# Kernel tuning notes

Measured on AMD Instinct MI355X. Metric: run time of the kernel, lower is better.

Reference implementation:

```python
import jax, jax.numpy as jnp
import numpy as np
from jax import lax

B, N, SEG, T = 64, 19, 15, 400
FIN, HID, K, NH, DM, FF, L, NC = 64, 128, 4, 4, 64, 128, 4, 3
EPS = 1e-5


def setup_inputs() -> dict:
    key = jax.random.key(0)
    ks = jax.random.split(key, 40)
    nrm = lambda i, s, sc=0.05: jax.random.normal(ks[i], s, dtype=jnp.float32) * sc
    inp = {
        "X": jax.random.normal(ks[0], (B, N, SEG, T), dtype=jnp.float32),
        "A_hat": jax.random.uniform(ks[1], (B, K, SEG, N, N), dtype=jnp.float32),
        "conv1_w": nrm(2, (32, 1, 25)), "conv1_b": nrm(3, (32,)),
        "conv2_w": nrm(4, (64, 32, 9)), "conv2_b": nrm(5, (64,)),
        "g1_W": nrm(6, (HID, FIN)), "g1_q": nrm(7, (K,), 1.0),
        "g1_bn_g": jnp.ones((HID,)), "g1_bn_b": jnp.zeros((HID,)),
        "g1_bn_m": jnp.zeros((HID,)), "g1_bn_v": jnp.ones((HID,)),
        "g2_W": nrm(8, (FIN, HID)), "g2_q": nrm(9, (K,), 1.0),
        "g2_bn_g": jnp.ones((FIN,)), "g2_bn_b": jnp.zeros((FIN,)),
        "g2_bn_m": jnp.zeros((FIN,)), "g2_bn_v": jnp.ones((FIN,)),
        "cls_token": nrm(10, (1, 1, DM), 0.02), "pos_emb": nrm(11, (1, SEG + 1, DM), 0.02),
        "t_wqkv": nrm(12, (L, 3 * DM, DM)), "t_bqkv": nrm(13, (L, 3 * DM)),
        "t_wo": nrm(14, (L, DM, DM)), "t_bo": nrm(15, (L, DM)),
        "t_ln1g": jnp.ones((L, DM)), "t_ln1b": jnp.zeros((L, DM)),
        "t_w1": nrm(16, (L, FF, DM)), "t_b1": nrm(17, (L, FF)),
        "t_w2": nrm(18, (L, DM, FF)), "t_b2": nrm(19, (L, DM)),
        "t_ln2g": jnp.ones((L, DM)), "t_ln2b": jnp.zeros((L, DM)),
        "clf_w": nrm(20, (NC, DM)), "clf_b": nrm(21, (NC,)),
    }
    return inp


def _ln(x, g, b):
    mu = x.mean(-1, keepdims=True)
    v = ((x - mu) ** 2).mean(-1, keepdims=True)
    return (x - mu) * lax.rsqrt(v + EPS) * g + b


def _maxpool(x, w):  # x: [M, C, T]
    return lax.reduce_window(x, -jnp.inf, lax.max, (1, 1, w), (1, 1, w), "VALID")


def _temporal_encoder(X, c1w, c1b, c2w, c2b):
    # X: [B, SEG, N, T] -> [B, SEG, N, FIN]
    x = X.reshape(-1, 1, T)
    dn = ("NCH", "OIH", "NCH")
    x = lax.conv_general_dilated(x, c1w, (4,), [(12, 12)], dimension_numbers=dn) + c1b[None, :, None]
    x = _maxpool(jax.nn.relu(x), 4)                      # [M,32,25]
    x = lax.conv_general_dilated(x, c2w, (2,), [(4, 4)], dimension_numbers=dn) + c2b[None, :, None]
    x = _maxpool(jax.nn.relu(x), 2)                      # [M,64,6]
    x = x.mean(-1)                                       # AdaptiveAvgPool1d(1)
    return x.reshape(B, SEG, N, FIN)


def _gcn(Xf, A, W, q, g, b, m, v):
    alpha = jax.nn.softmax(q)                            # [K]
    AX = jnp.einsum("bksnm,bsmf->bksnf", A, Xf)          # K-hop diffusion
    Hk = jnp.einsum("bksnf,of->bksno", AX, W)            # shared linear
    H = jnp.einsum("k,bksno->bsno", alpha, Hk)           # attn-weighted hop mix
    H = (H - m) * lax.rsqrt(v + EPS) * g + b             # eval-mode BatchNorm1d
    return jax.nn.relu(H)


def _forward(X, A_hat, conv1_w, conv1_b, conv2_w, conv2_b,
             g1_W, g1_q, g1_bn_g, g1_bn_b, g1_bn_m, g1_bn_v,
             g2_W, g2_q, g2_bn_g, g2_bn_b, g2_bn_m, g2_bn_v,
             cls_token, pos_emb, t_wqkv, t_bqkv, t_wo, t_bo,
             t_ln1g, t_ln1b, t_w1, t_b1, t_w2, t_b2, t_ln2g, t_ln2b,
             clf_w, clf_b):
    Xs = X.reshape(-1, N, SEG, T).transpose(0, 2, 1, 3)  # [B,SEG,N,T]
    feat = _temporal_encoder(Xs, conv1_w, conv1_b, conv2_w, conv2_b)
    H = _gcn(feat, A_hat, g1_W, g1_q, g1_bn_g, g1_bn_b, g1_bn_m, g1_bn_v)
    H = _gcn(H, A_hat, g2_W, g2_q, g2_bn_g, g2_bn_b, g2_bn_m, g2_bn_v)
    g = H.mean(axis=2)                                   # node-mean -> [B,SEG,DM]
    x = jnp.concatenate([jnp.broadcast_to(cls_token, (B, 1, DM)), g], axis=1)
    x = x + pos_emb[:, : SEG + 1]
    dh = DM // NH
    for l in range(L):
        qkv = x @ t_wqkv[l].T + t_bqkv[l]
        qh, kh, vh = [u.reshape(B, SEG + 1, NH, dh).transpose(0, 2, 1, 3)
                      for u in jnp.split(qkv, 3, axis=-1)]
        attn = jax.nn.softmax(jnp.einsum("bhqd,bhkd->bhqk", qh, kh) / jnp.sqrt(jnp.float32(dh)), axis=-1)
        o = jnp.einsum("bhqk,bhkd->bhqd", attn, vh).transpose(0, 2, 1, 3).reshape(B, SEG + 1, DM)
        x = _ln(x + o @ t_wo[l].T + t_bo[l], t_ln1g[l], t_ln1b[l])
        ff = jax.nn.relu(x @ t_w1[l].T + t_b1[l]) @ t_w2[l].T + t_b2[l]
        x = _ln(x + ff, t_ln2g[l], t_ln2b[l])
    return x[:, 0] @ clf_w.T + clf_b                     # [B, NC]


def reference(X, A_hat, conv1_w, conv1_b, conv2_w, conv2_b,
              g1_W, g1_q, g1_bn_g, g1_bn_b, g1_bn_m, g1_bn_v,
              g2_W, g2_q, g2_bn_g, g2_bn_b, g2_bn_m, g2_bn_v,
              cls_token, pos_emb, t_wqkv, t_bqkv, t_wo, t_bo,
              t_ln1g, t_ln1b, t_w1, t_b1, t_w2, t_b2, t_ln2g, t_ln2b,
              clf_w, clf_b):
    return _forward(X, A_hat, conv1_w, conv1_b, conv2_w, conv2_b,
                    g1_W, g1_q, g1_bn_g, g1_bn_b, g1_bn_m, g1_bn_v,
                    g2_W, g2_q, g2_bn_g, g2_bn_b, g2_bn_m, g2_bn_v,
                    cls_token, pos_emb, t_wqkv, t_bqkv, t_wo, t_bo,
                    t_ln1g, t_ln1b, t_w1, t_b1, t_w2, t_b2, t_ln2g, t_ln2b,
                    clf_w, clf_b)
```

## Files before the change

kernel.cpp:

```cpp
#include <hip/hip_runtime.h>
#include <cmath>

#define B_ 64
#define N_ 19
#define SEG_ 15
#define T_ 400
#define FIN_ 64
#define HID_ 128
#define K_ 4
#define NH_ 4
#define DM_ 64
#define FF_ 128
#define L_ 4
#define NC_ 3
#define EPS_ 1e-5f

typedef __attribute__((ext_vector_type(8))) short bf16x8;
typedef __attribute__((ext_vector_type(4))) short bf16x4;
typedef __attribute__((ext_vector_type(4))) float f32x4;
typedef unsigned short ushort_t;

__device__ __forceinline__ ushort_t f2bf(float x) {
  union { float f; unsigned u; } a; a.f = x;
  unsigned r = a.u + 0x7fffu + ((a.u >> 16) & 1u);
  return (ushort_t)(r >> 16);
}
__device__ __forceinline__ float bf2f(ushort_t h) {
  union { unsigned u; float f; } a; a.u = ((unsigned)h) << 16;
  return a.f;
}

__global__ __launch_bounds__(256) void k_prep(
    const float* __restrict__ c1w, const float* __restrict__ c2w,
    const float* __restrict__ wqkv, const float* __restrict__ wo,
    const float* __restrict__ w1, const float* __restrict__ w2,
    const float* __restrict__ g1W, const float* __restrict__ g2W,
    ushort_t* __restrict__ bt,
    ushort_t* __restrict__ Th, ushort_t* __restrict__ Tl,
    ushort_t* __restrict__ W1h, ushort_t* __restrict__ W1l,
    ushort_t* __restrict__ W2h, ushort_t* __restrict__ W2l,
    ushort_t* __restrict__ C1h, ushort_t* __restrict__ C1l) {
  int gid = blockIdx.x * 256 + threadIdx.x;
  if (gid < 18944) {
    int oc = gid / 296, k = gid - oc * 296;
    int ic = k & 31, kk = k >> 5;
    ushort_t v = 0;
    if (kk < 9) v = f2bf(c2w[oc * 288 + ic * 9 + kk]);
    bt[gid] = v;
  } else if (gid < 68096) {
    int i = gid - 18944;
    int l = i / 12288, r = i % 12288;
    float v = wqkv[i];
    ushort_t h = f2bf(v);
    int dst = l * 32768 + r;
    Th[dst] = h; Tl[dst] = f2bf(v - bf2f(h));
  } else if (gid < 84480) {
    int i = gid - 68096;
    int l = i / 4096, r = i % 4096;
    float v = wo[i];
    ushort_t h = f2bf(v);
    int dst = l * 32768 + 12288 + r;
    Th[dst] = h; Tl[dst] = f2bf(v - bf2f(h));
  } else if (gid < 117248) {
    int i = gid - 84480;
    int l = i / 8192, r = i % 8192;
    float v = w1[i];
    ushort_t h = f2bf(v);
    int dst = l * 32768 + 16384 + r;
    Th[dst] = h; Tl[dst] = f2bf(v - bf2f(h));
  } else if (gid < 150016) {
    int i = gid - 117248;
    int l = i / 8192, r = i % 8192;
    float v = w2[i];
    ushort_t h = f2bf(v);
    int dst = l * 32768 + 24576 + r;
    Th[dst] = h; Tl[dst] = f2bf(v - bf2f(h));
  } else if (gid < 158208) {
    int i = gid - 150016;
    float v = g1W[i];
    ushort_t h = f2bf(v);
    W1h[i] = h;
    W1l[i] = f2bf(v - bf2f(h));
  } else if (gid < 166400) {
    int i = gid - 158208;
    float v = g2W[i];
    ushort_t h = f2bf(v);
    W2h[i] = h;
    W2l[i] = f2bf(v - bf2f(h));
  } else if (gid < 167424) {
    int i = gid - 166400;
    int oc = i >> 5, kk = i & 31;
    float v = (kk < 25) ? c1w[oc * 25 + kk] : 0.f;
    ushort_t h = f2bf(v);
    C1h[i] = h;
    C1l[i] = f2bf(v - bf2f(h));
  }
}

#define RPB 4
#define ICP 40
#define P1R 40
#define OFF_XPH 0
#define OFF_XPL 3840
#define OFF_P1  7680
#define SMEM_T  20480

__global__ __launch_bounds__(256, 4) void k_temporal(
    const float* __restrict__ X, const float* __restrict__ c1b,
    const float* __restrict__ c2b,
    const ushort_t* __restrict__ C1h, const ushort_t* __restrict__ C1l,
    const ushort_t* __restrict__ BmatT, float* __restrict__ Xf) {
  __shared__ __align__(16) unsigned char smem[SMEM_T];
  ushort_t* xph = (ushort_t*)(smem + OFF_XPH);
  ushort_t* xpl = (ushort_t*)(smem + OFF_XPL);
  ushort_t* p1T = (ushort_t*)(smem + OFF_P1);
  float* Dbuf = (float*)smem;

  const int tid = threadIdx.x;
  const int row0 = blockIdx.x * RPB;
  const int lane = tid & 63, wv = tid >> 6;
  const int quad = lane >> 4, nl = lane & 15;

  for (int i = tid; i < 3200; i += 256) ((unsigned*)p1T)[i] = 0u;
  for (int r = 0; r < RPB; ++r) {
    const int gr = row0 + r;
    const int n = gr % N_;
    const int s = (gr / N_) % SEG_;
    const int b = gr / (N_ * SEG_);
    const float* xin = X + (((size_t)b * N_ + n) * SEG_ + s) * T_ - 12;
    for (int i = tid; i < 480; i += 256) {
      float v = (i >= 12 && i < 412) ? xin[i] : 0.f;
      ushort_t h = f2bf(v);
      xph[r * 480 + i] = h;
      xpl[r * 480 + i] = f2bf(v - bf2f(h));
    }
  }
  __syncthreads();

  {
    bf16x8 bh0 = *(const bf16x8*)(C1h + nl * 32 + quad * 8);
    bf16x8 bh1 = *(const bf16x8*)(C1h + (16 + nl) * 32 + quad * 8);
    bf16x8 bl0 = *(const bf16x8*)(C1l + nl * 32 + quad * 8);
    bf16x8 bl1 = *(const bf16x8*)(C1l + (16 + nl) * 32 + quad * 8);
    const float bias0 = c1b[nl], bias1 = c1b[16 + nl];
    for (int t = wv; t < 28; t += 4) {
      const int r = t / 7, mt = t - r * 7;
      const int aoff = r * 480 + mt * 64 + nl * 4 + quad * 8;
      union { bf16x4 q[2]; bf16x8 v; } ah, al;
      ah.q[0] = *(const bf16x4*)(xph + aoff);
      ah.q[1] = *(const bf16x4*)(xph + aoff + 4);
      al.q[0] = *(const bf16x4*)(xpl + aoff);
      al.q[1] = *(const bf16x4*)(xpl + aoff + 4);
      f32x4 a0 = (f32x4){0.f, 0.f, 0.f, 0.f};
      a0 = __builtin_amdgcn_mfma_f32_16x16x32_bf16(ah.v, bh0, a0, 0, 0, 0);
      a0 = __builtin_amdgcn_mfma_f32_16x16x32_bf16(al.v, bh0, a0, 0, 0, 0);
      a0 = __builtin_amdgcn_mfma_f32_16x16x32_bf16(ah.v, bl0, a0, 0, 0, 0);
      f32x4 a1 = (f32x4){0.f, 0.f, 0.f, 0.f};
      a1 = __builtin_amdgcn_mfma_f32_16x16x32_bf16(ah.v, bh1, a1, 0, 0, 0);
      a1 = __builtin_amdgcn_mfma_f32_16x16x32_bf16(al.v, bh1, a1, 0, 0, 0);
      a1 = __builtin_amdgcn_mfma_f32_16x16x32_bf16(ah.v, bl1, a1, 0, 0, 0);
      const int j = mt * 4 + quad;
      if (j < 25) {
        float m0 = fmaxf(fmaxf(a0[0], a0[1]), fmaxf(a0[2], a0[3]));
        float m1 = fmaxf(fmaxf(a1[0], a1[1]), fmaxf(a1[2], a1[3]));
        p1T[(r * P1R + j + 4) * ICP + nl] = f2bf(fmaxf(m0 + bias0, 0.f));
        p1T[(r * P1R + j + 4) * ICP + 16 + nl] = f2bf(fmaxf(m1 + bias1, 0.f));
      }
    }
  }
  __syncthreads();

  f32x4 acc[4];
  int abase[4];
#pragma unroll
  for (int tm = 0; tm < 4; ++tm) {
    acc[tm] = (f32x4){0.f, 0.f, 0.f, 0.f};
    int m = tm * 16 + nl;
    int rl = m / 14;
    int op = m - rl * 14;
    if (rl > 3) rl = 3;
    if (op > 13) op = 13;
    abase[tm] = (rl * P1R + 2 * op) * ICP + quad * 8;
  }
  const ushort_t* brow = BmatT + (wv * 16 + nl) * 296 + quad * 8;
#pragma unroll
  for (int kk = 0; kk < 9; ++kk) {
    bf16x8 bfr = *(const bf16x8*)(brow + kk * 32);
#pragma unroll
    for (int tm = 0; tm < 4; ++tm) {
      bf16x8 afr = *(const bf16x8*)(p1T + abase[tm] + kk * ICP);
      acc[tm] = __builtin_amdgcn_mfma_f32_16x16x32_bf16(afr, bfr, acc[tm], 0, 0, 0);
    }
  }
  __syncthreads();

#pragma unroll
  for (int tm = 0; tm < 4; ++tm)
#pragma unroll
    for (int rg = 0; rg < 4; ++rg)
      Dbuf[(tm * 16 + quad * 4 + rg) * 66 + wv * 16 + nl] = acc[tm][rg];
  __syncthreads();

  for (int o = tid; o < RPB * 64; o += 256) {
    int rl = o >> 6, oc = o & 63;
    float bias = c2b[oc];
    const float* dr = Dbuf + (rl * 14) * 66 + oc;
    float s = 0.f;
#pragma unroll
    for (int jj = 0; jj < 6; ++jj) {
      float v = fmaxf(dr[(2 * jj) * 66], dr[(2 * jj + 1) * 66]) + bias;
      s += fmaxf(v, 0.f);
    }
    Xf[(size_t)(row0 + rl) * FIN_ + oc] = s * (1.f / 6.f);
  }
}

__global__ __launch_bounds__(256, 2) void k_gcn(
    const float* __restrict__ A, const float* __restrict__ Xf,
    const ushort_t* __restrict__ W1h, const ushort_t* __restrict__ W1l,
    const ushort_t* __restrict__ W2h, const ushort_t* __restrict__ W2l,
    const float* __restrict__ q1, const float* __restrict__ q2,
    const float* __restrict__ b1g, const float* __restrict__ b1b,
    const float* __restrict__ b1m, const float* __restrict__ b1v,
    const float* __restrict__ b2g, const float* __restrict__ b2b,
    const float* __restrict__ b2m, const float* __restrict__ b2v,
    float* __restrict__ G) {
  const int bs = blockIdx.x;
  const int b = bs / SEG_;
  const int s = bs % SEG_;
  const int tid = threadIdx.x;
  const int lane = tid & 63, wv = tid >> 6;
  const int quad = lane >> 4, nl = lane & 15;

  __shared__ __align__(16) ushort_t xh[32 * 72], xl[32 * 72];
  __shared__ __align__(16) ushort_t Hh[32 * 136], Hl[32 * 136];
  __shared__ __align__(16) ushort_t a1h[32 * 40], a1l[32 * 40];
  __shared__ __align__(16) ushort_t a2h[32 * 40], a2l[32 * 40];
  __shared__ __align__(16) ushort_t yTh[128 * 40], yTl[128 * 40];
  __shared__ float zbuf[N_ * 64];
  __shared__ float sc1[HID_], sh1[HID_], sc2[FIN_], sh2[FIN_];

  for (int i = tid; i < 32 * 72 / 2; i += 256) {
    ((unsigned*)xh)[i] = 0u; ((unsigned*)xl)[i] = 0u;
  }
  for (int i = tid; i < 32 * 136 / 2; i += 256) {
    ((unsigned*)Hh)[i] = 0u; ((unsigned*)Hl)[i] = 0u;
  }
  for (int i = tid; i < 32 * 40 / 2; i += 256) {
    ((unsigned*)a1h)[i] = 0u; ((unsigned*)a1l)[i] = 0u;
    ((unsigned*)a2h)[i] = 0u; ((unsigned*)a2l)[i] = 0u;
  }
  for (int o = tid; o < HID_; o += 256) {
    float sc = b1g[o] * rsqrtf(b1v[o] + EPS_);
    sc1[o] = sc; sh1[o] = b1b[o] - b1m[o] * sc;
  }
  for (int o = tid; o < FIN_; o += 256) {
    float sc = b2g[o] * rsqrtf(b2v[o] + EPS_);
    sc2[o] = sc; sh2[o] = b2b[o] - b2m[o] * sc;
  }
  __syncthreads();

  {
    float p0 = q1[0], p1 = q1[1], p2 = q1[2], p3 = q1[3];
    float mx = fmaxf(fmaxf(p0, p1), fmaxf(p2, p3));
    float e0 = expf(p0 - mx), e1 = expf(p1 - mx), e2 = expf(p2 - mx), e3 = expf(p3 - mx);
    float inv = 1.f / (e0 + e1 + e2 + e3);
    float a0 = e0 * inv, a1 = e1 * inv, a2 = e2 * inv, a3 = e3 * inv;
    float r0 = q2[0], r1 = q2[1], r2 = q2[2], r3 = q2[3];
    float mx2 = fmaxf(fmaxf(r0, r1), fmaxf(r2, r3));
    float f0 = expf(r0 - mx2), f1 = expf(r1 - mx2), f2 = expf(r2 - mx2), f3 = expf(r3 - mx2);
    float inv2 = 1.f / (f0 + f1 + f2 + f3);
    float c0 = f0 * inv2, c1 = f1 * inv2, c2 = f2 * inv2, c3 = f3 * inv2;
    const size_t kstride = (size_t)SEG_ * N_ * N_;
    const float* Ab = A + ((size_t)b * K_ * SEG_ + s) * (N_ * N_);
    for (int i = tid; i < N_ * N_; i += 256) {
      int n = i / N_, m = i - n * N_;
      float v0 = Ab[i], v1 = Ab[i + kstride], v2 = Ab[i + 2 * kstride], v3 = Ab[i + 3 * kstride];
      float w1v = a0 * v0 + a1 * v1 + a2 * v2 + a3 * v3;
      float w2v = c0 * v0 + c1 * v1 + c2 * v2 + c3 * v3;
      ushort_t h1 = f2bf(w1v);
      a1h[n * 40 + m] = h1; a1l[n * 40 + m] = f2bf(w1v - bf2f(h1));
      ushort_t h2 = f2bf(w2v);
      a2h[n * 40 + m] = h2; a2l[n * 40 + m] = f2bf(w2v - bf2f(h2));
    }
  }
  {
    const float* xb = Xf + (size_t)bs * N_ * FIN_;
    for (int i = tid; i < N_ * FIN_; i += 256) {
      int r = i >> 6, f = i & 63;
      float v = xb[i];
      ushort_t h = f2bf(v);
      xh[r * 72 + f] = h;
      xl[r * 72 + f] = f2bf(v - bf2f(h));
    }
  }
  __syncthreads();

#pragma unroll
  for (int mtl = 0; mtl < 2; ++mtl) {
    const int om = (wv * 2 + mtl) * 16;
#pragma unroll
    for (int nt = 0; nt < 2; ++nt) {
      f32x4 acc = (f32x4){0.f, 0.f, 0.f, 0.f};
#pragma unroll
      for (int ks = 0; ks < 2; ++ks) {
        bf16x8 ah = *(const bf16x8*)(W1h + (om + nl) * 64 + ks * 32 + quad * 8);
        bf16x8 al = *(const bf16x8*)(W1l + (om + nl) * 64 + ks * 32 + quad * 8);
        bf16x8 bh = *(const bf16x8*)(xh + (nt * 16 + nl) * 72 + ks * 32 + quad * 8);
        bf16x8 bl = *(const bf16x8*)(xl + (nt * 16 + nl) * 72 + ks * 32 + quad * 8);
        acc = __builtin_amdgcn_mfma_f32_16x16x32_bf16(ah, bh, acc, 0, 0, 0);
        acc = __builtin_amdgcn_mfma_f32_16x16x32_bf16(al, bh, acc, 0, 0, 0);
        acc = __builtin_amdgcn_mfma_f32_16x16x32_bf16(ah, bl, acc, 0, 0, 0);
      }
#pragma unroll
      for (int r = 0; r < 4; ++r) {
        int o = om + quad * 4 + r, node = nt * 16 + nl;
        float v = acc[r];
        ushort_t hh = f2bf(v);
        yTh[o * 40 + node] = hh;
        yTl[o * 40 + node] = f2bf(v - bf2f(hh));
      }
    }
  }
  __syncthreads();

#pragma unroll
  for (int mt = 0; mt < 2; ++mt) {
#pragma unroll
    for (int ntl = 0; ntl < 2; ++ntl) {
      const int nt = wv * 2 + ntl;
      f32x4 acc = (f32x4){0.f, 0.f, 0.f, 0.f};
      bf16x8 ah = *(const bf16x8*)(a1h + (mt * 16 + nl) * 40 + quad * 8);
      bf16x8 al = *(const bf16x8*)(a1l + (mt * 16 + nl) * 40 + quad * 8);
      bf16x8 bh = *(const bf16x8*)(yTh + (nt * 16 + nl) * 40 + quad * 8);
      bf16x8 bl = *(const bf16x8*)(yTl + (nt * 16 + nl) * 40 + quad * 8);
      acc = __builtin_amdgcn_mfma_f32_16x16x32_bf16(ah, bh, acc, 0, 0, 0);
      acc = __builtin_amdgcn_mfma_f32_16x16x32_bf16(al, bh, acc, 0, 0, 0);
      acc = __builtin_amdgcn_mfma_f32_16x16x32_bf16(ah, bl, acc, 0, 0, 0);
      const int o = nt * 16 + nl;
      const float sc = sc1[o], sh = sh1[o];
#pragma unroll
      for (int r = 0; r < 4; ++r) {
        int node = mt * 16 + quad * 4 + r;
        if (node < N_) {
          float h = fmaxf(acc[r] * sc + sh, 0.f);
          ushort_t hh = f2bf(h);
          Hh[node * 136 + o] = hh;
          Hl[node * 136 + o] = f2bf(h - bf2f(hh));
        }
      }
    }
  }
  __syncthreads();

  {
    const int om = wv * 16;
#pragma unroll
    for (int nt = 0; nt < 2; ++nt) {
      f32x4 acc = (f32x4){0.f, 0.f, 0.f, 0.f};
#pragma unroll
      for (int ks = 0; ks < 4; ++ks) {
        bf16x8 ah = *(const bf16x8*)(W2h + (om + nl) * 128 + ks * 32 + quad * 8);
        bf16x8 al = *(const bf16x8*)(W2l + (om + nl) * 128 + ks * 32 + quad * 8);
        bf16x8 bh = *(const bf16x8*)(Hh + (nt * 16 + nl) * 136 + ks * 32 + quad * 8);
        bf16x8 bl = *(const bf16x8*)(Hl + (nt * 16 + nl) * 136 + ks * 32 + quad * 8);
        acc = __builtin_amdgcn_mfma_f32_16x16x32_bf16(ah, bh, acc, 0, 0, 0);
        acc = __builtin_amdgcn_mfma_f32_16x16x32_bf16(al, bh, acc, 0, 0, 0);
        acc = __builtin_amdgcn_mfma_f32_16x16x32_bf16(ah, bl, acc, 0, 0, 0);
      }
#pragma unroll
      for (int r = 0; r < 4; ++r) {
        int o2 = om + quad * 4 + r, node = nt * 16 + nl;
        float v = acc[r];
        ushort_t hh = f2bf(v);
        yTh[o2 * 40 + node] = hh;
        yTl[o2 * 40 + node] = f2bf(v - bf2f(hh));
      }
    }
  }
  __syncthreads();

#pragma unroll
  for (int mt = 0; mt < 2; ++mt) {
    f32x4 acc = (f32x4){0.f, 0.f, 0.f, 0.f};
    bf16x8 ah = *(const bf16x8*)(a2h + (mt * 16 + nl) * 40 + quad * 8);
    bf16x8 al = *(const bf16x8*)(a2l + (mt * 16 + nl) * 40 + quad * 8);
    bf16x8 bh = *(const bf16x8*)(yTh + (wv * 16 + nl) * 40 + quad * 8);
    bf16x8 bl = *(const bf16x8*)(yTl + (wv * 16 + nl) * 40 + quad * 8);
    acc = __builtin_amdgcn_mfma_f32_16x16x32_bf16(ah, bh, acc, 0, 0, 0);
    acc = __builtin_amdgcn_mfma_f32_16x16x32_bf16(al, bh, acc, 0, 0, 0);
    acc = __builtin_amdgcn_mfma_f32_16x16x32_bf16(ah, bl, acc, 0, 0, 0);
    const int o2 = wv * 16 + nl;
    const float sc = sc2[o2], sh = sh2[o2];
#pragma unroll
    for (int r = 0; r < 4; ++r) {
      int node = mt * 16 + quad * 4 + r;
      if (node < N_)
        zbuf[node * 64 + o2] = fmaxf(acc[r] * sc + sh, 0.f);
    }
  }
  __syncthreads();

  if (tid < FIN_) {
    float ssum = 0.f;
#pragma unroll
    for (int nn = 0; nn < N_; ++nn) ssum += zbuf[nn * 64 + tid];
    G[(size_t)bs * FIN_ + tid] = ssum * (1.f / (float)N_);
  }
}

__global__ __launch_bounds__(256, 1) void k_transformer(
    const float* __restrict__ G, const float* __restrict__ cls,
    const float* __restrict__ pos,
    const ushort_t* __restrict__ Th, const ushort_t* __restrict__ Tl,
    const float* __restrict__ bqkv, const float* __restrict__ bo,
    const float* __restrict__ ln1g, const float* __restrict__ ln1b,
    const float* __restrict__ b1, const float* __restrict__ b2,
    const float* __restrict__ ln2g, const float* __restrict__ ln2b,
    const float* __restrict__ clfw, const float* __restrict__ clfb,
    float* __restrict__ out) {
  const int b = blockIdx.x;
  const int tid = threadIdx.x;
  const int lane = tid & 63, wv = tid >> 6;
  const int quad = lane >> 4, nl = lane & 15;

  __shared__ float xbuf[16 * 64];
  __shared__ __align__(16) ushort_t xh[16 * 72], xl[16 * 72];
  __shared__ float qkvb[16 * 196];
  __shared__ float scb[NH_ * 272];
  __shared__ __align__(16) ushort_t oh[16 * 72], ol[16 * 72];
  __shared__ __align__(16) ushort_t h1h[16 * 136], h1l[16 * 136];
  __shared__ float tmpb[16 * 64];
  __shared__ __align__(16) float pbuf[L_ * 704];
  __shared__ __align__(16) float cw[200];

  for (int i = tid; i < L_ * 704; i += 256) {
    int l = i / 704, r = i - l * 704;
    float v;
    if (r < 192)       v = bqkv[l * 192 + r];
    else if (r < 256)  v = bo[l * 64 + r - 192];
    else if (r < 384)  v = b1[l * 128 + r - 256];
    else if (r < 448)  v = b2[l * 64 + r - 384];
    else if (r < 512)  v = ln1g[l * 64 + r - 448];
    else if (r < 576)  v = ln1b[l * 64 + r - 512];
    else if (r < 640)  v = ln2g[l * 64 + r - 576];
    else               v = ln2b[l * 64 + r - 640];
    pbuf[i] = v;
  }
  if (tid < 192) cw[tid] = clfw[tid];
  if (tid < NC_) cw[192 + tid] = clfb[tid];

  for (int i = tid; i < 16 * 64; i += 256) {
    int t = i >> 6, d = i & 63;
    float base = (t == 0) ? cls[d] : G[((size_t)b * SEG_ + (t - 1)) * DM_ + d];
    float v = base + pos[t * DM_ + d];
    xbuf[i] = v;
    ushort_t h = f2bf(v);
    xh[t * 72 + d] = h;
    xl[t * 72 + d] = f2bf(v - bf2f(h));
  }
  __syncthreads();

  for (int l = 0; l < L_; ++l) {
    const ushort_t* TH = Th + l * 32768;
    const ushort_t* TL = Tl + l * 32768;
    const float* P = pbuf + l * 704;

    bf16x8 qwh[3][2], qwl[3][2];
#pragma unroll
    for (int ntl = 0; ntl < 3; ++ntl)
#pragma unroll
      for (int ks = 0; ks < 2; ++ks) {
        const int nt = wv * 3 + ntl;
        qwh[ntl][ks] = *(const bf16x8*)(TH + (nt * 16 + nl) * 64 + ks * 32 + quad * 8);
        qwl[ntl][ks] = *(const bf16x8*)(TL + (nt * 16 + nl) * 64 + ks * 32 + quad * 8);
      }
    bf16x8 owh[2], owl[2];
#pragma unroll
    for (int ks = 0; ks < 2; ++ks) {
      owh[ks] = *(const bf16x8*)(TH + 12288 + (wv * 16 + nl) * 64 + ks * 32 + quad * 8);
      owl[ks] = *(const bf16x8*)(TL + 12288 + (wv * 16 + nl) * 64 + ks * 32 + quad * 8);
    }
    bf16x8 f1h[2][2], f1l[2][2];
#pragma unroll
    for (int ntl = 0; ntl < 2; ++ntl)
#pragma unroll
      for (int ks = 0; ks < 2; ++ks) {
        const int nt = wv * 2 + ntl;
        f1h[ntl][ks] = *(const bf16x8*)(TH + 16384 + (nt * 16 + nl) * 64 + ks * 32 + quad * 8);
        f1l[ntl][ks] = *(const bf16x8*)(TL + 16384 + (nt * 16 + nl) * 64 + ks * 32 + quad * 8);
      }
    bf16x8 f2h[4], f2l[4];
#pragma unroll
    for (int ks = 0; ks < 4; ++ks) {
      f2h[ks] = *(const bf16x8*)(TH + 24576 + (wv * 16 + nl) * 128 + ks * 32 + quad * 8);
      f2l[ks] = *(const bf16x8*)(TL + 24576 + (wv * 16 + nl) * 128 + ks * 32 + quad * 8);
    }

#pragma unroll
    for (int ntl = 0; ntl < 3; ++ntl) {
      const int nt = wv * 3 + ntl;
      f32x4 acc = (f32x4){0.f, 0.f, 0.f, 0.f};
#pragma unroll
      for (int ks = 0; ks < 2; ++ks) {
        bf16x8 ah = *(const bf16x8*)(xh + nl * 72 + ks * 32 + quad * 8);
        bf16x8 al = *(const bf16x8*)(xl + nl * 72 + ks * 32 + quad * 8);
        acc = __builtin_amdgcn_mfma_f32_16x16x32_bf16(ah, qwh[ntl][ks], acc, 0, 0, 0);
        acc = __builtin_amdgcn_mfma_f32_16x16x32_bf16(al, qwh[ntl][ks], acc, 0, 0, 0);
        acc = __builtin_amdgcn_mfma_f32_16x16x32_bf16(ah, qwl[ntl][ks], acc, 0, 0, 0);
      }
      const int j = nt * 16 + nl;
      const float bias = P[j];
#pragma unroll
      for (int r = 0; r < 4; ++r)
        qkvb[(quad * 4 + r) * 196 + j] = acc[r] + bias;
    }
    __syncthreads();

    {
      const int h = wv;
      float sc[4];
      const float* qr = &qkvb[nl * 196 + h * 16];
#pragma unroll
      for (int uu = 0; uu < 4; ++uu) {
        const float* kr = &qkvb[(quad * 4 + uu) * 196 + 64 + h * 16];
        float a = 0.f;
#pragma unroll
        for (int d = 0; d < 16; ++d) a += qr[d] * kr[d];
        sc[uu] = a * 0.25f;
      }
      float mx = fmaxf(fmaxf(sc[0], sc[1]), fmaxf(sc[2], sc[3]));
      mx = fmaxf(mx, __shfl_xor(mx, 16));
      mx = fmaxf(mx, __shfl_xor(mx, 32));
      float e[4];
      float sum = 0.f;
#pragma unroll
      for (int uu = 0; uu < 4; ++uu) { e[uu] = expf(sc[uu] - mx); sum += e[uu]; }
      sum += __shfl_xor(sum, 16);
      sum += __shfl_xor(sum, 32);
      const float is = 1.f / sum;
      float* prow = &scb[h * 272 + nl * 17];
#pragma unroll
      for (int uu = 0; uu < 4; ++uu) prow[quad * 4 + uu] = e[uu] * is;
      float o[4] = {0.f, 0.f, 0.f, 0.f};
      for (int u = 0; u < 16; ++u) {
        float p = prow[u];
        const float* vr = &qkvb[u * 196 + 128 + h * 16 + quad * 4];
#pragma unroll
        for (int dd = 0; dd < 4; ++dd) o[dd] += p * vr[dd];
      }
      const int eb = h * 16 + quad * 4;
#pragma unroll
      for (int dd = 0; dd < 4; ++dd) {
        ushort_t hh = f2bf(o[dd]);
        oh[nl * 72 + eb + dd] = hh;
        ol[nl * 72 + eb + dd] = f2bf(o[dd] - bf2f(hh));
      }
    }
    __syncthreads();

    {
      f32x4 acc = (f32x4){0.f, 0.f, 0.f, 0.f};
#pragma unroll
      for (int ks = 0; ks < 2; ++ks) {
        bf16x8 ah = *(const bf16x8*)(oh + nl * 72 + ks * 32 + quad * 8);
        bf16x8 al = *(const bf16x8*)(ol + nl * 72 + ks * 32 + quad * 8);
        acc = __builtin_amdgcn_mfma_f32_16x16x32_bf16(ah, owh[ks], acc, 0, 0, 0);
        acc = __builtin_amdgcn_mfma_f32_16x16x32_bf16(al, owh[ks], acc, 0, 0, 0);
        acc = __builtin_amdgcn_mfma_f32_16x16x32_bf16(ah, owl[ks], acc, 0, 0, 0);
      }
      const int d = wv * 16 + nl;
      const float bias = P[192 + d];
#pragma unroll
      for (int r = 0; r < 4; ++r) {
        int t = quad * 4 + r;
        tmpb[t * 64 + d] = xbuf[t * 64 + d] + acc[r] + bias;
      }
    }
    __syncthreads();

    {
      int t = tid >> 4, i2 = tid & 15;
      float4 v = ((const float4*)(tmpb + t * 64))[i2];
      float s = v.x + v.y + v.z + v.w;
      s += __shfl_xor(s, 1); s += __shfl_xor(s, 2);
      s += __shfl_xor(s, 4); s += __shfl_xor(s, 8);
      float mu = s * (1.f / 64.f);
      float d0 = v.x - mu, d1 = v.y - mu, d2 = v.z - mu, d3 = v.w - mu;
      float vr = d0 * d0 + d1 * d1 + d2 * d2 + d3 * d3;
      vr += __shfl_xor(vr, 1); vr += __shfl_xor(vr, 2);
      vr += __shfl_xor(vr, 4); vr += __shfl_xor(vr, 8);
      float rs = rsqrtf(vr * (1.f / 64.f) + EPS_);
      float4 g4 = ((const float4*)(P + 448))[i2];
      float4 b4 = ((const float4*)(P + 512))[i2];
      float4 o4;
      o4.x = d0 * rs * g4.x + b4.x; o4.y = d1 * rs * g4.y + b4.y;
      o4.z = d2 * rs * g4.z + b4.z; o4.w = d3 * rs * g4.w + b4.w;
      ((float4*)(xbuf + t * 64))[i2] = o4;
      int base = t * 72 + i2 * 4;
      ushort_t h0 = f2bf(o4.x), h1 = f2bf(o4.y), h2 = f2bf(o4.z), h3 = f2bf(o4.w);
      xh[base + 0] = h0; xh[base + 1] = h1; xh[base + 2] = h2; xh[base + 3] = h3;
      xl[base + 0] = f2bf(o4.x - bf2f(h0));
      xl[base + 1] = f2bf(o4.y - bf2f(h1));
      xl[base + 2] = f2bf(o4.z - bf2f(h2));
      xl[base + 3] = f2bf(o4.w - bf2f(h3));
    }
    __syncthreads();

#pragma unroll
    for (int ntl = 0; ntl < 2; ++ntl) {
      const int nt = wv * 2 + ntl;
      f32x4 acc = (f32x4){0.f, 0.f, 0.f, 0.f};
#pragma unroll
      for (int ks = 0; ks < 2; ++ks) {
        bf16x8 ah = *(const bf16x8*)(xh + nl * 72 + ks * 32 + quad * 8);
        bf16x8 al = *(const bf16x8*)(xl + nl * 72 + ks * 32 + quad * 8);
        acc = __builtin_amdgcn_mfma_f32_16x16x32_bf16(ah, f1h[ntl][ks], acc, 0, 0, 0);
        acc = __builtin_amdgcn_mfma_f32_16x16x32_bf16(al, f1h[ntl][ks], acc, 0, 0, 0);
        acc = __builtin_amdgcn_mfma_f32_16x16x32_bf16(ah, f1l[ntl][ks], acc, 0, 0, 0);
      }
      const int f = nt * 16 + nl;
      const float bias = P[256 + f];
#pragma unroll
      for (int r = 0; r < 4; ++r) {
        int t = quad * 4 + r;
        float v = fmaxf(acc[r] + bias, 0.f);
        ushort_t hh = f2bf(v);
        h1h[t * 136 + f] = hh;
        h1l[t * 136 + f] = f2bf(v - bf2f(hh));
      }
    }
    __syncthreads();

    {
      f32x4 acc = (f32x4){0.f, 0.f, 0.f, 0.f};
#pragma unroll
      for (int ks = 0; ks < 4; ++ks) {
        bf16x8 ah = *(const bf16x8*)(h1h + nl * 136 + ks * 32 + quad * 8);
        bf16x8 al = *(const bf16x8*)(h1l + nl * 136 + ks * 32 + quad * 8);
        acc = __builtin_amdgcn_mfma_f32_16x16x32_bf16(ah, f2h[ks], acc, 0, 0, 0);
        acc = __builtin_amdgcn_mfma_f32_16x16x32_bf16(al, f2h[ks], acc, 0, 0, 0);
        acc = __builtin_amdgcn_mfma_f32_16x16x32_bf16(ah, f2l[ks], acc, 0, 0, 0);
      }
      const int d = wv * 16 + nl;
      const float bias = P[384 + d];
#pragma unroll
      for (int r = 0; r < 4; ++r) {
        int t = quad * 4 + r;
        tmpb[t * 64 + d] = xbuf[t * 64 + d] + acc[r] + bias;
      }
    }
    __syncthreads();

    {
      int t = tid >> 4, i2 = tid & 15;
      float4 v = ((const float4*)(tmpb + t * 64))[i2];
      float s = v.x + v.y + v.z + v.w;
      s += __shfl_xor(s, 1); s += __shfl_xor(s, 2);
      s += __shfl_xor(s, 4); s += __shfl_xor(s, 8);
      float mu = s * (1.f / 64.f);
      float d0 = v.x - mu, d1 = v.y - mu, d2 = v.z - mu, d3 = v.w - mu;
      float vr = d0 * d0 + d1 * d1 + d2 * d2 + d3 * d3;
      vr += __shfl_xor(vr, 1); vr += __shfl_xor(vr, 2);
      vr += __shfl_xor(vr, 4); vr += __shfl_xor(vr, 8);
      float rs = rsqrtf(vr * (1.f / 64.f) + EPS_);
      float4 g4 = ((const float4*)(P + 576))[i2];
      float4 b4 = ((const float4*)(P + 640))[i2];
      float4 o4;
      o4.x = d0 * rs * g4.x + b4.x; o4.y = d1 * rs * g4.y + b4.y;
      o4.z = d2 * rs * g4.z + b4.z; o4.w = d3 * rs * g4.w + b4.w;
      ((float4*)(xbuf + t * 64))[i2] = o4;
      int base = t * 72 + i2 * 4;
      ushort_t h0 = f2bf(o4.x), h1 = f2bf(o4.y), h2 = f2bf(o4.z), h3 = f2bf(o4.w);
      xh[base + 0] = h0; xh[base + 1] = h1; xh[base + 2] = h2; xh[base + 3] = h3;
      xl[base + 0] = f2bf(o4.x - bf2f(h0));
      xl[base + 1] = f2bf(o4.y - bf2f(h1));
      xl[base + 2] = f2bf(o4.z - bf2f(h2));
      xl[base + 3] = f2bf(o4.w - bf2f(h3));
    }
    __syncthreads();
  }

  if (tid < NC_) {
    float acc = cw[192 + tid];
    const float* wr = &cw[tid * DM_];
    for (int d = 0; d < DM_; ++d) acc += xbuf[d] * wr[d];
    out[b * NC_ + tid] = acc;
  }
}

extern "C" void kernel_launch(void* const* d_in, const int* in_sizes, int n_in,
                              void* d_out, int out_size, void* d_ws, size_t ws_size,
                              hipStream_t stream) {
  (void)in_sizes; (void)n_in; (void)out_size; (void)ws_size;
  const float* X    = (const float*)d_in[0];
  const float* A    = (const float*)d_in[1];
  const float* c1w  = (const float*)d_in[2];
  const float* c1b  = (const float*)d_in[3];
  const float* c2w  = (const float*)d_in[4];
  const float* c2b  = (const float*)d_in[5];
  const float* g1W  = (const float*)d_in[6];
  const float* g1q  = (const float*)d_in[7];
  const float* g1g  = (const float*)d_in[8];
  const float* g1b  = (const float*)d_in[9];
  const float* g1m  = (const float*)d_in[10];
  const float* g1v  = (const float*)d_in[11];
  const float* g2W  = (const float*)d_in[12];
  const float* g2q  = (const float*)d_in[13];
  const float* g2g  = (const float*)d_in[14];
  const float* g2b  = (const float*)d_in[15];
  const float* g2m  = (const float*)d_in[16];
  const float* g2v  = (const float*)d_in[17];
  const float* cls  = (const float*)d_in[18];
  const float* pos  = (const float*)d_in[19];
  const float* wqkv = (const float*)d_in[20];
  const float* bqkv = (const float*)d_in[21];
  const float* wo   = (const float*)d_in[22];
  const float* bo   = (const float*)d_in[23];
  const float* ln1g = (const float*)d_in[24];
  const float* ln1b = (const float*)d_in[25];
  const float* w1   = (const float*)d_in[26];
  const float* b1   = (const float*)d_in[27];
  const float* w2   = (const float*)d_in[28];
  const float* b2   = (const float*)d_in[29];
  const float* ln2g = (const float*)d_in[30];
  const float* ln2b = (const float*)d_in[31];
  const float* clfw = (const float*)d_in[32];
  const float* clfb = (const float*)d_in[33];
  float* out = (float*)d_out;

  char* wsb = (char*)d_ws;
  ushort_t* BmatT = (ushort_t*)(wsb + 0);
  ushort_t* Th  = (ushort_t*)(wsb + 37888);
  ushort_t* Tl  = (ushort_t*)(wsb + 300032);
  ushort_t* W1h = (ushort_t*)(wsb + 562176);
  ushort_t* W1l = (ushort_t*)(wsb + 578560);
  ushort_t* W2h = (ushort_t*)(wsb + 594944);
  ushort_t* W2l = (ushort_t*)(wsb + 611328);
  ushort_t* C1h = (ushort_t*)(wsb + 627712);
  ushort_t* C1l = (ushort_t*)(wsb + 629760);
  float* Xf   = (float*)(wsb + 631808);
  float* G    = (float*)(wsb + 5301248);

  k_prep<<<654, 256, 0, stream>>>(c1w, c2w, wqkv, wo, w1, w2, g1W, g2W,
                                  BmatT, Th, Tl, W1h, W1l, W2h, W2l, C1h, C1l);
  k_temporal<<<B_ * SEG_ * N_ / RPB, 256, 0, stream>>>(
      X, c1b, c2b, C1h, C1l, BmatT, Xf);
  k_gcn<<<B_ * SEG_, 256, 0, stream>>>(A, Xf, W1h, W1l, W2h, W2l,
                                       g1q, g2q, g1g, g1b, g1m, g1v,
                                       g2g, g2b, g2m, g2v, G);
  k_transformer<<<B_, 256, 0, stream>>>(G, cls, pos, Th, Tl,
                                        bqkv, bo, ln1g, ln1b, b1, b2, ln2g, ln2b,
                                        clfw, clfb, out);
}
```

Before: 221.8 us.

## Run transformer kernel as a single wavefront per batch, removing block barriers

The transformer kernel now launches one 64-lane wavefront per batch element instead of four waves. Every stage (QKV, per-head attention, output projection, layernorms, FFN) loops over all tiles and heads inside that one wave, so all __syncthreads are dropped. The shared-memory staging of biases and layernorm parameters is removed in favour of direct global reads, and the per-layer weight register prefetch is replaced by loads inside the MFMA loops. In exchange, each block now does four times the serial work with only 64 of the GPU's CUs busy and less latency hiding, so the serial MFMA chain and global weight loads may dominate.

```diff
diff --git a/kernel.cpp b/kernel.cpp
--- a/kernel.cpp
+++ b/kernel.cpp
@@ -409,7 +409,7 @@
   }
 }
 
-__global__ __launch_bounds__(256, 1) void k_transformer(
+__global__ __launch_bounds__(64, 1) void k_transformer(
     const float* __restrict__ G, const float* __restrict__ cls,
     const float* __restrict__ pos,
     const ushort_t* __restrict__ Th, const ushort_t* __restrict__ Tl,
@@ -420,113 +420,73 @@
     const float* __restrict__ clfw, const float* __restrict__ clfb,
     float* __restrict__ out) {
   const int b = blockIdx.x;
-  const int tid = threadIdx.x;
-  const int lane = tid & 63, wv = tid >> 6;
+  const int lane = threadIdx.x;
   const int quad = lane >> 4, nl = lane & 15;
 
   __shared__ float xbuf[16 * 64];
   __shared__ __align__(16) ushort_t xh[16 * 72], xl[16 * 72];
   __shared__ float qkvb[16 * 196];
-  __shared__ float scb[NH_ * 272];
+  __shared__ float scb[16 * 17];
   __shared__ __align__(16) ushort_t oh[16 * 72], ol[16 * 72];
   __shared__ __align__(16) ushort_t h1h[16 * 136], h1l[16 * 136];
   __shared__ float tmpb[16 * 64];
-  __shared__ __align__(16) float pbuf[L_ * 704];
-  __shared__ __align__(16) float cw[200];
-
-  for (int i = tid; i < L_ * 704; i += 256) {
-    int l = i / 704, r = i - l * 704;
-    float v;
-    if (r < 192)       v = bqkv[l * 192 + r];
-    else if (r < 256)  v = bo[l * 64 + r - 192];
-    else if (r < 384)  v = b1[l * 128 + r - 256];
-    else if (r < 448)  v = b2[l * 64 + r - 384];
-    else if (r < 512)  v = ln1g[l * 64 + r - 448];
-    else if (r < 576)  v = ln1b[l * 64 + r - 512];
-    else if (r < 640)  v = ln2g[l * 64 + r - 576];
-    else               v = ln2b[l * 64 + r - 640];
-    pbuf[i] = v;
-  }
-  if (tid < 192) cw[tid] = clfw[tid];
-  if (tid < NC_) cw[192 + tid] = clfb[tid];
-
-  for (int i = tid; i < 16 * 64; i += 256) {
-    int t = i >> 6, d = i & 63;
-    float base = (t == 0) ? cls[d] : G[((size_t)b * SEG_ + (t - 1)) * DM_ + d];
-    float v = base + pos[t * DM_ + d];
-    xbuf[i] = v;
-    ushort_t h = f2bf(v);
-    xh[t * 72 + d] = h;
-    xl[t * 72 + d] = f2bf(v - bf2f(h));
-  }
-  __syncthreads();
+
+#pragma unroll
+  for (int g = 0; g < 4; ++g) {
+    const int t = g * 4 + quad;
+    float4 base = (t == 0) ? ((const float4*)cls)[nl]
+                           : ((const float4*)(G + ((size_t)b * SEG_ + (t - 1)) * DM_))[nl];
+    float4 p = ((const float4*)(pos + t * DM_))[nl];
+    float4 v;
+    v.x = base.x + p.x; v.y = base.y + p.y;
+    v.z = base.z + p.z; v.w = base.w + p.w;
+    ((float4*)(xbuf + t * 64))[nl] = v;
+    const int bi = t * 72 + nl * 4;
+    ushort_t h0 = f2bf(v.x), h1 = f2bf(v.y), h2 = f2bf(v.z), h3 = f2bf(v.w);
+    xh[bi + 0] = h0; xh[bi + 1] = h1; xh[bi + 2] = h2; xh[bi + 3] = h3;
+    xl[bi + 0] = f2bf(v.x - bf2f(h0));
+    xl[bi + 1] = f2bf(v.y - bf2f(h1));
+    xl[bi + 2] = f2bf(v.z - bf2f(h2));
+    xl[bi + 3] = f2bf(v.w - bf2f(h3));
+  }
 
   for (int l = 0; l < L_; ++l) {
     const ushort_t* TH = Th + l * 32768;
     const ushort_t* TL = Tl + l * 32768;
-    const float* P = pbuf + l * 704;
-
-    bf16x8 qwh[3][2], qwl[3][2];
-#pragma unroll
-    for (int ntl = 0; ntl < 3; ++ntl)
-#pragma unroll
-      for (int ks = 0; ks < 2; ++ks) {
-        const int nt = wv * 3 + ntl;
-        qwh[ntl][ks] = *(const bf16x8*)(TH + (nt * 16 + nl) * 64 + ks * 32 + quad * 8);
-        qwl[ntl][ks] = *(const bf16x8*)(TL + (nt * 16 + nl) * 64 + ks * 32 + quad * 8);
-      }
-    bf16x8 owh[2], owl[2];
-#pragma unroll
-    for (int ks = 0; ks < 2; ++ks) {
-      owh[ks] = *(const bf16x8*)(TH + 12288 + (wv * 16 + nl) * 64 + ks * 32 + quad * 8);
-      owl[ks] = *(const bf16x8*)(TL + 12288 + (wv * 16 + nl) * 64 + ks * 32 + quad * 8);
-    }
-    bf16x8 f1h[2][2], f1l[2][2];
-#pragma unroll
-    for (int ntl = 0; ntl < 2; ++ntl)
-#pragma unroll
-      for (int ks = 0; ks < 2; ++ks) {
-        const int nt = wv * 2 + ntl;
-        f1h[ntl][ks] = *(const bf16x8*)(TH + 16384 + (nt * 16 + nl) * 64 + ks * 32 + quad * 8);
-        f1l[ntl][ks] = *(const bf16x8*)(TL + 16384 + (nt * 16 + nl) * 64 + ks * 32 + quad * 8);
-      }
-    bf16x8 f2h[4], f2l[4];
-#pragma unroll
-    for (int ks = 0; ks < 4; ++ks) {
-      f2h[ks] = *(const bf16x8*)(TH + 24576 + (wv * 16 + nl) * 128 + ks * 32 + quad * 8);
-      f2l[ks] = *(const bf16x8*)(TL + 24576 + (wv * 16 + nl) * 128 + ks * 32 + quad * 8);
-    }
-
-#pragma unroll
-    for (int ntl = 0; ntl < 3; ++ntl) {
-      const int nt = wv * 3 + ntl;
+
+#pragma unroll
+    for (int nt = 0; nt < 12; ++nt) {
       f32x4 acc = (f32x4){0.f, 0.f, 0.f, 0.f};
 #pragma unroll
       for (int ks = 0; ks < 2; ++ks) {
         bf16x8 ah = *(const bf16x8*)(xh + nl * 72 + ks * 32 + quad * 8);
         bf16x8 al = *(const bf16x8*)(xl + nl * 72 + ks * 32 + quad * 8);
-        acc = __builtin_amdgcn_mfma_f32_16x16x32_bf16(ah, qwh[ntl][ks], acc, 0, 0, 0);
-        acc = __builtin_amdgcn_mfma_f32_16x16x32_bf16(al, qwh[ntl][ks], acc, 0, 0, 0);
-        acc = __builtin_amdgcn_mfma_f32_16x16x32_bf16(ah, qwl[ntl][ks], acc, 0, 0, 0);
+        bf16x8 bh = *(const bf16x8*)(TH + (nt * 16 + nl) * 64 + ks * 32 + quad * 8);
+        bf16x8 bl = *(const bf16x8*)(TL + (nt * 16 + nl) * 64 + ks * 32 + quad * 8);
+        acc = __builtin_amdgcn_mfma_f32_16x16x32_bf16(ah, bh, acc, 0, 0, 0);
+        acc = __builtin_amdgcn_mfma_f32_16x16x32_bf16(al, bh, acc, 0, 0, 0);
+        acc = __builtin_amdgcn_mfma_f32_16x16x32_bf16(ah, bl, acc, 0, 0, 0);
       }
       const int j = nt * 16 + nl;
-      const float bias = P[j];
+      const float bias = bqkv[l * 192 + j];
 #pragma unroll
       for (int r = 0; r < 4; ++r)
         qkvb[(quad * 4 + r) * 196 + j] = acc[r] + bias;
     }
-    __syncthreads();
-
-    {
-      const int h = wv;
+
+#pragma unroll
+    for (int h = 0; h < NH_; ++h) {
       float sc[4];
-      const float* qr = &qkvb[nl * 196 + h * 16];
+      const float4* qr = (const float4*)(qkvb + nl * 196 + h * 16);
+      float4 q0 = qr[0], q1 = qr[1], q2 = qr[2], q3 = qr[3];
 #pragma unroll
       for (int uu = 0; uu < 4; ++uu) {
-        const float* kr = &qkvb[(quad * 4 + uu) * 196 + 64 + h * 16];
-        float a = 0.f;
-#pragma unroll
-        for (int d = 0; d < 16; ++d) a += qr[d] * kr[d];
+        const float4* kr = (const float4*)(qkvb + (quad * 4 + uu) * 196 + 64 + h * 16);
+        float4 k0 = kr[0], k1 = kr[1], k2 = kr[2], k3 = kr[3];
+        float a = q0.x * k0.x + q0.y * k0.y + q0.z * k0.z + q0.w * k0.w
+                + q1.x * k1.x + q1.y * k1.y + q1.z * k1.z + q1.w * k1.w
+                + q2.x * k2.x + q2.y * k2.y + q2.z * k2.z + q2.w * k2.w
+                + q3.x * k3.x + q3.y * k3.y + q3.z * k3.z + q3.w * k3.w;
         sc[uu] = a * 0.25f;
       }
       float mx = fmaxf(fmaxf(sc[0], sc[1]), fmaxf(sc[2], sc[3]));
@@ -539,49 +499,51 @@
       sum += __shfl_xor(sum, 16);
       sum += __shfl_xor(sum, 32);
       const float is = 1.f / sum;
-      float* prow = &scb[h * 272 + nl * 17];
+      float* prow = &scb[nl * 17];
 #pragma unroll
       for (int uu = 0; uu < 4; ++uu) prow[quad * 4 + uu] = e[uu] * is;
-      float o[4] = {0.f, 0.f, 0.f, 0.f};
+      float o0 = 0.f, o1 = 0.f, o2 = 0.f, o3 = 0.f;
+#pragma unroll
       for (int u = 0; u < 16; ++u) {
         float p = prow[u];
-        const float* vr = &qkvb[u * 196 + 128 + h * 16 + quad * 4];
-#pragma unroll
-        for (int dd = 0; dd < 4; ++dd) o[dd] += p * vr[dd];
-      }
-      const int eb = h * 16 + quad * 4;
-#pragma unroll
-      for (int dd = 0; dd < 4; ++dd) {
-        ushort_t hh = f2bf(o[dd]);
-        oh[nl * 72 + eb + dd] = hh;
-        ol[nl * 72 + eb + dd] = f2bf(o[dd] - bf2f(hh));
-      }
-    }
-    __syncthreads();
-
-    {
+        float4 vv = *(const float4*)(qkvb + u * 196 + 128 + h * 16 + quad * 4);
+        o0 += p * vv.x; o1 += p * vv.y; o2 += p * vv.z; o3 += p * vv.w;
+      }
+      const int eb = nl * 72 + h * 16 + quad * 4;
+      ushort_t h0 = f2bf(o0), h1 = f2bf(o1), h2 = f2bf(o2), h3 = f2bf(o3);
+      oh[eb + 0] = h0; oh[eb + 1] = h1; oh[eb + 2] = h2; oh[eb + 3] = h3;
+      ol[eb + 0] = f2bf(o0 - bf2f(h0));
+      ol[eb + 1] = f2bf(o1 - bf2f(h1));
+      ol[eb + 2] = f2bf(o2 - bf2f(h2));
+      ol[eb + 3] = f2bf(o3 - bf2f(h3));
+    }
+
+#pragma unroll
+    for (int nt = 0; nt < 4; ++nt) {
       f32x4 acc = (f32x4){0.f, 0.f, 0.f, 0.f};
 #pragma unroll
       for (int ks = 0; ks < 2; ++ks) {
         bf16x8 ah = *(const bf16x8*)(oh + nl * 72 + ks * 32 + quad * 8);
         bf16x8 al = *(const bf16x8*)(ol + nl * 72 + ks * 32 + quad * 8);
-        acc = __builtin_amdgcn_mfma_f32_16x16x32_bf16(ah, owh[ks], acc, 0, 0, 0);
-        acc = __builtin_amdgcn_mfma_f32_16x16x32_bf16(al, owh[ks], acc, 0, 0, 0);
-        acc = __builtin_amdgcn_mfma_f32_16x16x32_bf16(ah, owl[ks], acc, 0, 0, 0);
-      }
-      const int d = wv * 16 + nl;
-      const float bias = P[192 + d];
+        bf16x8 bh = *(const bf16x8*)(TH + 12288 + (nt * 16 + nl) * 64 + ks * 32 + quad * 8);
+        bf16x8 bl = *(const bf16x8*)(TL + 12288 + (nt * 16 + nl) * 64 + ks * 32 + quad * 8);
+        acc = __builtin_amdgcn_mfma_f32_16x16x32_bf16(ah, bh, acc, 0, 0, 0);
+        acc = __builtin_amdgcn_mfma_f32_16x16x32_bf16(al, bh, acc, 0, 0, 0);
+        acc = __builtin_amdgcn_mfma_f32_16x16x32_bf16(ah, bl, acc, 0, 0, 0);
+      }
+      const int d = nt * 16 + nl;
+      const float bias = bo[l * 64 + d];
 #pragma unroll
       for (int r = 0; r < 4; ++r) {
         int t = quad * 4 + r;
         tmpb[t * 64 + d] = xbuf[t * 64 + d] + acc[r] + bias;
       }
     }
-    __syncthreads();
-
-    {
-      int t = tid >> 4, i2 = tid & 15;
-      float4 v = ((const float4*)(tmpb + t * 64))[i2];
+
+#pragma unroll
+    for (int g = 0; g < 4; ++g) {
+      const int t = g * 4 + quad;
+      float4 v = ((const float4*)(tmpb + t * 64))[nl];
       float s = v.x + v.y + v.z + v.w;
       s += __shfl_xor(s, 1); s += __shfl_xor(s, 2);
       s += __shfl_xor(s, 4); s += __shfl_xor(s, 8);
@@ -591,36 +553,36 @@
       vr += __shfl_xor(vr, 1); vr += __shfl_xor(vr, 2);
       vr += __shfl_xor(vr, 4); vr += __shfl_xor(vr, 8);
       float rs = rsqrtf(vr * (1.f / 64.f) + EPS_);
-      float4 g4 = ((const float4*)(P + 448))[i2];
-      float4 b4 = ((const float4*)(P + 512))[i2];
+      float4 g4 = ((const float4*)(ln1g + l * 64))[nl];
+      float4 b4 = ((const float4*)(ln1b + l * 64))[nl];
       float4 o4;
       o4.x = d0 * rs * g4.x + b4.x; o4.y = d1 * rs * g4.y + b4.y;
       o4.z = d2 * rs * g4.z + b4.z; o4.w = d3 * rs * g4.w + b4.w;
-      ((float4*)(xbuf + t * 64))[i2] = o4;
-      int base = t * 72 + i2 * 4;
+      ((float4*)(xbuf + t * 64))[nl] = o4;
+      const int bi = t * 72 + nl * 4;
       ushort_t h0 = f2bf(o4.x), h1 = f2bf(o4.y), h2 = f2bf(o4.z), h3 = f2bf(o4.w);
-      xh[base + 0] = h0; xh[base + 1] = h1; xh[base + 2] = h2; xh[base + 3] = h3;
-      xl[base + 0] = f2bf(o4.x - bf2f(h0));
-      xl[base + 1] = f2bf(o4.y - bf2f(h1));
-      xl[base + 2] = f2bf(o4.z - bf2f(h2));
-      xl[base + 3] = f2bf(o4.w - bf2f(h3));
-    }
-    __syncthreads();
-
-#pragma unroll
-    for (int ntl = 0; ntl < 2; ++ntl) {
-      const int nt = wv * 2 + ntl;
+      xh[bi + 0] = h0; xh[bi + 1] = h1; xh[bi + 2] = h2; xh[bi + 3] = h3;
+      xl[bi + 0] = f2bf(o4.x - bf2f(h0));
+      xl[bi + 1] = f2bf(o4.y - bf2f(h1));
+      xl[bi + 2] = f2bf(o4.z - bf2f(h2));
+      xl[bi + 3] = f2bf(o4.w - bf2f(h3));
+    }
+
+#pragma unroll
+    for (int nt = 0; nt < 8; ++nt) {
       f32x4 acc = (f32x4){0.f, 0.f, 0.f, 0.f};
 #pragma unroll
       for (int ks = 0; ks < 2; ++ks) {
         bf16x8 ah = *(const bf16x8*)(xh + nl * 72 + ks * 32 + quad * 8);
         bf16x8 al = *(const bf16x8*)(xl + nl * 72 + ks * 32 + quad * 8);
-        acc = __builtin_amdgcn_mfma_f32_16x16x32_bf16(ah, f1h[ntl][ks], acc, 0, 0, 0);
-        acc = __builtin_amdgcn_mfma_f32_16x16x32_bf16(al, f1h[ntl][ks], acc, 0, 0, 0);
-        acc = __builtin_amdgcn_mfma_f32_16x16x32_bf16(ah, f1l[ntl][ks], acc, 0, 0, 0);
+        bf16x8 bh = *(const bf16x8*)(TH + 16384 + (nt * 16 + nl) * 64 + ks * 32 + quad * 8);
+        bf16x8 bl = *(const bf16x8*)(TL + 16384 + (nt * 16 + nl) * 64 + ks * 32 + quad * 8);
+        acc = __builtin_amdgcn_mfma_f32_16x16x32_bf16(ah, bh, acc, 0, 0, 0);
+        acc = __builtin_amdgcn_mfma_f32_16x16x32_bf16(al, bh, acc, 0, 0, 0);
+        acc = __builtin_amdgcn_mfma_f32_16x16x32_bf16(ah, bl, acc, 0, 0, 0);
       }
       const int f = nt * 16 + nl;
-      const float bias = P[256 + f];
+      const float bias = b1[l * 128 + f];
 #pragma unroll
       for (int r = 0; r < 4; ++r) {
         int t = quad * 4 + r;
@@ -630,31 +592,33 @@
         h1l[t * 136 + f] = f2bf(v - bf2f(hh));
       }
     }
-    __syncthreads();
-
-    {
+
+#pragma unroll
+    for (int nt = 0; nt < 4; ++nt) {
       f32x4 acc = (f32x4){0.f, 0.f, 0.f, 0.f};
 #pragma unroll
       for (int ks = 0; ks < 4; ++ks) {
         bf16x8 ah = *(const bf16x8*)(h1h + nl * 136 + ks * 32 + quad * 8);
         bf16x8 al = *(const bf16x8*)(h1l + nl * 136 + ks * 32 + quad * 8);
-        acc = __builtin_amdgcn_mfma_f32_16x16x32_bf16(ah, f2h[ks], acc, 0, 0, 0);
-        acc = __builtin_amdgcn_mfma_f32_16x16x32_bf16(al, f2h[ks], acc, 0, 0, 0);
-        acc = __builtin_amdgcn_mfma_f32_16x16x32_bf16(ah, f2l[ks], acc, 0, 0, 0);
-      }
-      const int d = wv * 16 + nl;
-      const float bias = P[384 + d];
+        bf16x8 bh = *(const bf16x8*)(TH + 24576 + (nt * 16 + nl) * 128 + ks * 32 + quad * 8);
+        bf16x8 bl = *(const bf16x8*)(TL + 24576 + (nt * 16 + nl) * 128 + ks * 32 + quad * 8);
+        acc = __builtin_amdgcn_mfma_f32_16x16x32_bf16(ah, bh, acc, 0, 0, 0);
+        acc = __builtin_amdgcn_mfma_f32_16x16x32_bf16(al, bh, acc, 0, 0, 0);
+        acc = __builtin_amdgcn_mfma_f32_16x16x32_bf16(ah, bl, acc, 0, 0, 0);
+      }
+      const int d = nt * 16 + nl;
+      const float bias = b2[l * 64 + d];
 #pragma unroll
       for (int r = 0; r < 4; ++r) {
         int t = quad * 4 + r;
         tmpb[t * 64 + d] = xbuf[t * 64 + d] + acc[r] + bias;
       }
     }
-    __syncthreads();
-
-    {
-      int t = tid >> 4, i2 = tid & 15;
-      float4 v = ((const float4*)(tmpb + t * 64))[i2];
+
+#pragma unroll
+    for (int g = 0; g < 4; ++g) {
+      const int t = g * 4 + quad;
+      float4 v = ((const float4*)(tmpb + t * 64))[nl];
       float s = v.x + v.y + v.z + v.w;
       s += __shfl_xor(s, 1); s += __shfl_xor(s, 2);
       s += __shfl_xor(s, 4); s += __shfl_xor(s, 8);
@@ -664,28 +628,27 @@
       vr += __shfl_xor(vr, 1); vr += __shfl_xor(vr, 2);
       vr += __shfl_xor(vr, 4); vr += __shfl_xor(vr, 8);
       float rs = rsqrtf(vr * (1.f / 64.f) + EPS_);
-      float4 g4 = ((const float4*)(P + 576))[i2];
-      float4 b4 = ((const float4*)(P + 640))[i2];
+      float4 g4 = ((const float4*)(ln2g + l * 64))[nl];
+      float4 b4 = ((const float4*)(ln2b + l * 64))[nl];
       float4 o4;
       o4.x = d0 * rs * g4.x + b4.x; o4.y = d1 * rs * g4.y + b4.y;
       o4.z = d2 * rs * g4.z + b4.z; o4.w = d3 * rs * g4.w + b4.w;
-      ((float4*)(xbuf + t * 64))[i2] = o4;
-      int base = t * 72 + i2 * 4;
+      ((float4*)(xbuf + t * 64))[nl] = o4;
+      const int bi = t * 72 + nl * 4;
       ushort_t h0 = f2bf(o4.x), h1 = f2bf(o4.y), h2 = f2bf(o4.z), h3 = f2bf(o4.w);
-      xh[base + 0] = h0; xh[base + 1] = h1; xh[base + 2] = h2; xh[base + 3] = h3;
-      xl[base + 0] = f2bf(o4.x - bf2f(h0));
-      xl[base + 1] = f2bf(o4.y - bf2f(h1));
-      xl[base + 2] = f2bf(o4.z - bf2f(h2));
-      xl[base + 3] = f2bf(o4.w - bf2f(h3));
-    }
-    __syncthreads();
-  }
-
-  if (tid < NC_) {
-    float acc = cw[192 + tid];
-    const float* wr = &cw[tid * DM_];
+      xh[bi + 0] = h0; xh[bi + 1] = h1; xh[bi + 2] = h2; xh[bi + 3] = h3;
+      xl[bi + 0] = f2bf(o4.x - bf2f(h0));
+      xl[bi + 1] = f2bf(o4.y - bf2f(h1));
+      xl[bi + 2] = f2bf(o4.z - bf2f(h2));
+      xl[bi + 3] = f2bf(o4.w - bf2f(h3));
+    }
+  }
+
+  if (lane < NC_) {
+    float acc = clfb[lane];
+    const float* wr = &clfw[lane * DM_];
     for (int d = 0; d < DM_; ++d) acc += xbuf[d] * wr[d];
-    out[b * NC_ + tid] = acc;
+    out[b * NC_ + lane] = acc;
   }
 }
 
@@ -749,7 +712,7 @@
   k_gcn<<<B_ * SEG_, 256, 0, stream>>>(A, Xf, W1h, W1l, W2h, W2l,
                                        g1q, g2q, g1g, g1b, g1m, g1v,
                                        g2g, g2b, g2m, g2v, G);
-  k_transformer<<<B_, 256, 0, stream>>>(G, cls, pos, Th, Tl,
-                                        bqkv, bo, ln1g, ln1b, b1, b2, ln2g, ln2b,
-                                        clfw, clfb, out);
+  k_transformer<<<B_, 64, 0, stream>>>(G, cls, pos, Th, Tl,
+                                       bqkv, bo, ln1g, ln1b, b1, b2, ln2g, ln2b,
+                                       clfw, clfb, out);
 }
```

Result: slower. 245.6 us (+10.8%).
